# Kernel optimization log

Measured on AMD Instinct MI355X. Metric: run time of the kernel, lower is better.

Reference implementation:

```python
import jax, jax.numpy as jnp
import numpy as np

CHANNELS = 256
HEADS = 8
GROUPS = 32
EPS = 1e-5


def setup_inputs() -> dict:
    key = jax.random.key(0)
    ks = jax.random.split(key, 9)
    c = CHANNELS
    s = 1.0 / np.sqrt(c)
    return {
        "x": jax.random.normal(ks[0], (2, c, 64, 64), dtype=jnp.float32),
        "gn_w": jnp.ones((c,), jnp.float32),
        "gn_b": jnp.zeros((c,), jnp.float32),
        "qkv_w": jax.random.normal(ks[1], (3 * c, c), jnp.float32) * s,
        "qkv_b": jnp.zeros((3 * c,), jnp.float32),
        "proj_w": jax.random.normal(ks[2], (c, c), jnp.float32) * s,
        "proj_b": jnp.zeros((c,), jnp.float32),
        "gproj_w": jax.random.normal(ks[3], (c, c), jnp.float32) * s,
        "gproj_b": jnp.zeros((c,), jnp.float32),
    }


def reference(x, gn_w, gn_b, qkv_w, qkv_b, proj_w, proj_b, gproj_w, gproj_b):
    b, c, h, w = x.shape
    n = h * w
    hd = c // HEADS
    scale = hd ** (-0.5)

    # GroupNorm(32, c)
    xg = x.reshape(b, GROUPS, -1)
    mu = jnp.mean(xg, axis=-1, keepdims=True)
    var = jnp.mean((xg - mu) ** 2, axis=-1, keepdims=True)
    xn = ((xg - mu) * jax.lax.rsqrt(var + EPS)).reshape(b, c, h, w)
    xn = xn * gn_w[None, :, None, None] + gn_b[None, :, None, None]

    # global context: AdaptiveAvgPool2d(1) + 1x1 conv -> [b, c]
    gfeat = jnp.mean(xn, axis=(2, 3))                      # [b, c]
    gfeat = gfeat @ gproj_w.T + gproj_b                    # [b, c]

    # qkv 1x1 conv
    qkv = jnp.einsum('bchw,oc->bohw', xn, qkv_w) + qkv_b[None, :, None, None]
    q, k, v = qkv[:, :c], qkv[:, c:2 * c], qkv[:, 2 * c:]

    q = q.reshape(b, HEADS, hd, n).transpose(0, 1, 3, 2)   # [b,H,N,d]
    k = k.reshape(b, HEADS, hd, n) + gfeat.reshape(b, HEADS, hd, 1) * 0.1  # [b,H,d,N]
    v = v.reshape(b, HEADS, hd, n).transpose(0, 1, 3, 2)   # [b,H,N,d]

    attn = jax.nn.softmax(jnp.einsum('bhnd,bhdm->bhnm', q, k) * scale, axis=-1)
    out = jnp.einsum('bhnm,bhmd->bhnd', attn, v)           # [b,H,N,d]
    out = out.transpose(0, 1, 3, 2).reshape(b, c, h, w)

    out = jnp.einsum('bchw,oc->bohw', out, proj_w) + proj_b[None, :, None, None]
    out = out + gfeat[:, :, None, None] * 0.1
    return out + x
```

## Files before the change

kernel.cpp:

```cpp
#include <hip/hip_runtime.h>
#include <hip/hip_bf16.h>
#include <stdint.h>

#define BATCH 2
#define CH 256
#define NSP 4096
#define HEADS 8
#define HD 32
#define GROUPS 32
#define EPS_GN 1e-5f
#define NSPLIT 4

#define ATT_SCALE (0.17677669529663687f * 1.4426950408889634f)

typedef __attribute__((ext_vector_type(8))) short short8;
typedef __attribute__((ext_vector_type(4))) float f32x4;
typedef __attribute__((ext_vector_type(16))) float f32x16;
typedef __attribute__((ext_vector_type(2))) float f32x2;

#define ZERO16 ((f32x16){0.f,0.f,0.f,0.f,0.f,0.f,0.f,0.f,0.f,0.f,0.f,0.f,0.f,0.f,0.f,0.f})

static __device__ __forceinline__ unsigned short f2bf(float f) {
    union { float f; unsigned u; } v; v.f = f;
    unsigned r = v.u + 0x7fffu + ((v.u >> 16) & 1u);
    return (unsigned short)(r >> 16);
}
static __device__ __forceinline__ unsigned pkbf(float x, float y) {
    __hip_bfloat162 h = __float22bfloat162_rn(make_float2(x, y));
    return *(unsigned*)&h;
}

__global__ void k_gnstats(const float* __restrict__ x, float* __restrict__ stats) {
    int bg = blockIdx.x;
    int t = threadIdx.x;
    const float4* b4 = (const float4*)(x + (size_t)bg * (8 * NSP));
    float s = 0.f, sq = 0.f;
    #pragma unroll
    for (int i = 0; i < 32; i++) {
        float4 v = b4[t + i * 256];
        s  += v.x + v.y + v.z + v.w;
        sq += v.x * v.x + v.y * v.y + v.z * v.z + v.w * v.w;
    }
    #pragma unroll
    for (int off = 32; off > 0; off >>= 1) {
        s  += __shfl_down(s, off);
        sq += __shfl_down(sq, off);
    }
    __shared__ float rs[4], rq[4];
    int w = t >> 6;
    if ((t & 63) == 0) { rs[w] = s; rq[w] = sq; }
    __syncthreads();
    if (t == 0) {
        float S = rs[0] + rs[1] + rs[2] + rs[3];
        float Q = rq[0] + rq[1] + rq[2] + rq[3];
        float mu  = S * (1.0f / 32768.0f);
        float var = Q * (1.0f / 32768.0f) - mu * mu;
        stats[bg * 2]     = mu;
        stats[bg * 2 + 1] = rsqrtf(var + EPS_GN);
    }
}

__global__ void k_gnapply(const float* __restrict__ x, const float* __restrict__ gn_w,
                          const float* __restrict__ gn_b, const float* __restrict__ stats,
                          unsigned short* __restrict__ xnt, float* __restrict__ gpart) {
    int p0 = blockIdx.x * 64, c0 = blockIdx.y * 64, b = blockIdx.z;
    int t = threadIdx.x;
    __shared__ float tile[64][65];
    int ci0 = t >> 4, pq = t & 15;
    #pragma unroll
    for (int k = 0; k < 4; k++) {
        int ci = ci0 + k * 16;
        int c = c0 + ci;
        float mu   = stats[(b * GROUPS + (c >> 3)) * 2];
        float rstd = stats[(b * GROUPS + (c >> 3)) * 2 + 1];
        float w  = gn_w[c] * rstd;
        float bb = gn_b[c] - mu * w;
        float4 v = *(const float4*)(x + ((size_t)(b * CH + c)) * NSP + p0 + pq * 4);
        tile[ci][pq * 4 + 0] = v.x * w + bb;
        tile[ci][pq * 4 + 1] = v.y * w + bb;
        tile[ci][pq * 4 + 2] = v.z * w + bb;
        tile[ci][pq * 4 + 3] = v.w * w + bb;
    }
    __syncthreads();
    int pi = t >> 2, cb = (t & 3) * 16;
    unsigned pack[8];
    #pragma unroll
    for (int e = 0; e < 8; e++) {
        float a  = tile[cb + 2 * e][pi];
        float bv = tile[cb + 2 * e + 1][pi];
        pack[e] = (unsigned)f2bf(a) | ((unsigned)f2bf(bv) << 16);
    }
    uint4* dst = (uint4*)(xnt + ((size_t)(b * NSP + p0 + pi)) * CH + c0 + cb);
    dst[0] = make_uint4(pack[0], pack[1], pack[2], pack[3]);
    dst[1] = make_uint4(pack[4], pack[5], pack[6], pack[7]);
    if (t < 64) {
        float s = 0.f;
        #pragma unroll
        for (int j = 0; j < 64; j++) s += tile[t][j];
        gpart[((size_t)(b * CH + c0 + t)) * 64 + blockIdx.x] = s;
    }
}

__global__ void k_gproj(const float* __restrict__ gpart, const float* __restrict__ gproj_w,
                        const float* __restrict__ gproj_b, float* __restrict__ gfeat) {
    int b = blockIdx.x, t = threadIdx.x;
    __shared__ float graw[256];
    const float* p = gpart + ((size_t)(b * CH + t)) * 64;
    float s = 0.f;
    #pragma unroll
    for (int i = 0; i < 64; i++) s += p[i];
    graw[t] = s * (1.0f / 4096.0f);
    __syncthreads();
    float acc = gproj_b[t];
    const float* wr = gproj_w + (size_t)t * CH;
    #pragma unroll 8
    for (int c = 0; c < 256; c++) acc += graw[c] * wr[c];
    gfeat[b * CH + t] = acc;
}

__global__ void k_convert(const float* __restrict__ qkv_w, const float* __restrict__ proj_w,
                          unsigned short* __restrict__ wbf) {
    int i4 = blockIdx.x * 256 + threadIdx.x;
    const float* src = (i4 < 49152) ? (qkv_w + (size_t)i4 * 4)
                                    : (proj_w + (size_t)(i4 - 49152) * 4);
    float4 v = *(const float4*)src;
    ushort4 o;
    o.x = f2bf(v.x); o.y = f2bf(v.y); o.z = f2bf(v.z); o.w = f2bf(v.w);
    *(ushort4*)(wbf + (size_t)i4 * 4) = o;
}

__global__ void k_gemm_qkv(const unsigned short* __restrict__ Ag,
                           const unsigned short* __restrict__ Btg,
                           const float* __restrict__ bias,
                           const float* __restrict__ gfeat,
                           unsigned short* __restrict__ qt,
                           unsigned short* __restrict__ kt,
                           unsigned short* __restrict__ vt) {
    int n0 = blockIdx.x * 128, m0 = blockIdx.y * 64, b = blockIdx.z;
    int t = threadIdx.x, lane = t & 63, w = t >> 6;
    int wm = w >> 1, wn = w & 1;
    __shared__ short A_lds[64][40];
    __shared__ short B_lds[128][40];
    const unsigned short* Bb = Btg + (size_t)b * NSP * CH;
    f32x4 acc[2][4];
    #pragma unroll
    for (int m = 0; m < 2; m++)
        #pragma unroll
        for (int n = 0; n < 4; n++) acc[m][n] = (f32x4){0.f, 0.f, 0.f, 0.f};
    int arow = t >> 2, akk = (t & 3) * 8;
    for (int k0 = 0; k0 < 256; k0 += 32) {
        __syncthreads();
        *(uint4*)&A_lds[arow][akk] = *(const uint4*)(Ag + (size_t)(m0 + arow) * CH + k0 + akk);
        #pragma unroll
        for (int hh = 0; hh < 2; hh++) {
            int f = t + hh * 256;
            int j = f >> 2, kk = (f & 3) * 8;
            *(uint4*)&B_lds[j][kk] = *(const uint4*)(Bb + (size_t)(n0 + j) * CH + k0 + kk);
        }
        __syncthreads();
        short8 a[2], bf[4];
        #pragma unroll
        for (int m = 0; m < 2; m++)
            a[m] = *(const short8*)&A_lds[wm * 32 + m * 16 + (lane & 15)][(lane >> 4) * 8];
        #pragma unroll
        for (int n = 0; n < 4; n++)
            bf[n] = *(const short8*)&B_lds[wn * 64 + n * 16 + (lane & 15)][(lane >> 4) * 8];
        #pragma unroll
        for (int m = 0; m < 2; m++)
            #pragma unroll
            for (int n = 0; n < 4; n++)
                acc[m][n] = __builtin_amdgcn_mfma_f32_16x16x32_bf16(a[m], bf[n], acc[m][n], 0, 0, 0);
    }
    int rbase = m0 + wm * 32 + ((lane >> 4) << 2);
    int cbase = n0 + wn * 64 + (lane & 15);
    #pragma unroll
    for (int m = 0; m < 2; m++) {
        int row0 = rbase + m * 16;
        int sec = row0 >> 8;
        int ch  = row0 & 255;
        int h = ch >> 5, d0 = ch & 31;
        #pragma unroll
        for (int n = 0; n < 4; n++) {
            int col = cbase + n * 16;
            if (sec == 0) {
                ushort4 pk;
                pk.x = f2bf(acc[m][n][0] + bias[row0 + 0]);
                pk.y = f2bf(acc[m][n][1] + bias[row0 + 1]);
                pk.z = f2bf(acc[m][n][2] + bias[row0 + 2]);
                pk.w = f2bf(acc[m][n][3] + bias[row0 + 3]);
                *(ushort4*)(qt + ((size_t)((b * 8 + h) * NSP + col)) * HD + d0) = pk;
            } else if (sec == 1) {
                ushort4 pk;
                #pragma unroll
                for (int i = 0; i < 4; i++) {
                    float v = (acc[m][n][i] + bias[row0 + i]
                               + 0.1f * gfeat[b * CH + ch + i]) * ATT_SCALE;
                    ((unsigned short*)&pk)[i] = f2bf(v);
                }
                *(ushort4*)(kt + ((size_t)((b * 8 + h) * NSP + col)) * HD + d0) = pk;
            } else {
                #pragma unroll
                for (int i = 0; i < 4; i++) {
                    float v = acc[m][n][i] + bias[row0 + i];
                    vt[((size_t)((b * 8 + h) * HD + d0 + i)) * NSP + col] = f2bf(v);
                }
            }
        }
    }
}

__global__ void k_gemm_proj(const unsigned short* __restrict__ Ag,
                            const unsigned short* __restrict__ Btg,
                            const float* __restrict__ bias,
                            const float* __restrict__ gfeat,
                            const float* __restrict__ xres,
                            float* __restrict__ out) {
    int n0 = blockIdx.x * 128, m0 = blockIdx.y * 64, b = blockIdx.z;
    int t = threadIdx.x, lane = t & 63, w = t >> 6;
    int wm = w >> 1, wn = w & 1;
    __shared__ short A_lds[64][40];
    __shared__ short B_lds[128][40];
    const unsigned short* Bb = Btg + (size_t)b * NSP * CH;
    f32x4 acc[2][4];
    #pragma unroll
    for (int m = 0; m < 2; m++)
        #pragma unroll
        for (int n = 0; n < 4; n++) acc[m][n] = (f32x4){0.f, 0.f, 0.f, 0.f};
    int arow = t >> 2, akk = (t & 3) * 8;
    for (int k0 = 0; k0 < 256; k0 += 32) {
        __syncthreads();
        *(uint4*)&A_lds[arow][akk] = *(const uint4*)(Ag + (size_t)(m0 + arow) * CH + k0 + akk);
        #pragma unroll
        for (int hh = 0; hh < 2; hh++) {
            int f = t + hh * 256;
            int j = f >> 2, kk = (f & 3) * 8;
            *(uint4*)&B_lds[j][kk] = *(const uint4*)(Bb + (size_t)(n0 + j) * CH + k0 + kk);
        }
        __syncthreads();
        short8 a[2], bf[4];
        #pragma unroll
        for (int m = 0; m < 2; m++)
            a[m] = *(const short8*)&A_lds[wm * 32 + m * 16 + (lane & 15)][(lane >> 4) * 8];
        #pragma unroll
        for (int n = 0; n < 4; n++)
            bf[n] = *(const short8*)&B_lds[wn * 64 + n * 16 + (lane & 15)][(lane >> 4) * 8];
        #pragma unroll
        for (int m = 0; m < 2; m++)
            #pragma unroll
            for (int n = 0; n < 4; n++)
                acc[m][n] = __builtin_amdgcn_mfma_f32_16x16x32_bf16(a[m], bf[n], acc[m][n], 0, 0, 0);
    }
    int rbase = m0 + wm * 32 + ((lane >> 4) << 2);
    int cbase = n0 + wn * 64 + (lane & 15);
    #pragma unroll
    for (int m = 0; m < 2; m++) {
        #pragma unroll
        for (int n = 0; n < 4; n++) {
            int col = cbase + n * 16;
            #pragma unroll
            for (int i = 0; i < 4; i++) {
                int row = rbase + m * 16 + i;
                float add = bias[row] + 0.1f * gfeat[b * CH + row]
                          + xres[((size_t)(b * CH + row)) * NSP + col];
                out[((size_t)(b * CH + row)) * NSP + col] = acc[m][n][i] + add;
            }
        }
    }
}

__global__ __launch_bounds__(256, 8)
void k_flash32(const unsigned short* __restrict__ qt,
               const unsigned short* __restrict__ kt,
               const unsigned short* __restrict__ vt,
               unsigned short* __restrict__ opart, float* __restrict__ lpart) {
    const int h = blockIdx.y, b = blockIdx.z;
    const int s = blockIdx.x >> 5;
    const int t = threadIdx.x, lane = t & 63, w = t >> 6;
    const int lo32 = lane & 31, hi = lane >> 5;
    const int q0 = (blockIdx.x & 31) * 128 + w * 32;
    const int j0base = s * (NSP / NSPLIT);
    const unsigned short* qp = qt + ((size_t)(b * 8 + h) * NSP) * HD;
    const unsigned short* kp = kt + ((size_t)(b * 8 + h) * NSP) * HD;
    const unsigned short* vp = vt + ((size_t)(b * 8 + h) * HD) * NSP;
    __shared__ __align__(16) unsigned short K_lds[64 * 40];
    __shared__ __align__(16) unsigned short V_lds[32 * 64];

    short8 qf0 = *(const short8*)(qp + (size_t)(q0 + lo32) * HD + hi * 8);
    short8 qf1 = *(const short8*)(qp + (size_t)(q0 + lo32) * HD + 16 + hi * 8);
    f32x16 oacc;
    #pragma unroll
    for (int i = 0; i < 16; i++) oacc[i] = 0.f;
    float l = 0.f;

    const int krow = (t & 7) + 8 * (t >> 5);
    const int kslot = (t >> 3) & 3;
    const int vd = t >> 3, vslot = t & 7;
    const unsigned short* kga = kp + (size_t)(j0base + krow) * HD + kslot * 8;
    const unsigned short* vga = vp + (size_t)vd * NSP + j0base + vslot * 8;
    const int kws = krow * 40 + kslot * 8;
    const int vws = vd * 64 + ((vslot ^ (vd & 7)) * 8);

    const int NT = NSP / NSPLIT / 64;
    for (int it = 0; it < NT; ++it) {
        {
            uint4 kreg = *(const uint4*)(kga + (size_t)it * 64 * HD);
            uint4 vreg = *(const uint4*)(vga + it * 64);
            *(uint4*)&K_lds[kws] = kreg;
            *(uint4*)&V_lds[vws] = vreg;
        }
        __syncthreads();
        #pragma unroll
        for (int hf = 0; hf < 2; hf++) {
            const int jj = hf * 32 + lo32;
            short8 kf0 = *(const short8*)&K_lds[jj * 40 + hi * 8];
            short8 kf1 = *(const short8*)&K_lds[jj * 40 + (2 + hi) * 8];
            f32x16 sv;
            __builtin_amdgcn_s_setprio(1);
            sv = __builtin_amdgcn_mfma_f32_32x32x16_bf16(kf0, qf0, ZERO16, 0, 0, 0);
            sv = __builtin_amdgcn_mfma_f32_32x32x16_bf16(kf1, qf1, sv, 0, 0, 0);
            __builtin_amdgcn_s_setprio(0);
            #pragma unroll
            for (int i = 0; i < 16; i++) sv[i] = __builtin_amdgcn_exp2f(sv[i]);
            {
                #define SH2(V, I) __builtin_shufflevector(V, V, 2*(I), 2*(I)+1)
                f32x2 t0 = (SH2(sv,0) + SH2(sv,1)) + (SH2(sv,2) + SH2(sv,3));
                f32x2 t1 = (SH2(sv,4) + SH2(sv,5)) + (SH2(sv,6) + SH2(sv,7));
                f32x2 tt = t0 + t1;
                float sm = tt[0] + tt[1];
                #undef SH2
                unsigned sb = __builtin_bit_cast(unsigned, sm);
                auto sx = __builtin_amdgcn_permlane32_swap(sb, sb, false, false);
                l += __builtin_bit_cast(float, (unsigned)sx[0])
                   + __builtin_bit_cast(float, (unsigned)sx[1]);
            }
            #define PVSTEP(SV, BB, C) { \
                unsigned p0 = pkbf(SV[BB + 0], SV[BB + 1]); \
                unsigned p1 = pkbf(SV[BB + 2], SV[BB + 3]); \
                unsigned p2 = pkbf(SV[BB + 4], SV[BB + 5]); \
                unsigned p3 = pkbf(SV[BB + 6], SV[BB + 7]); \
                auto s02 = __builtin_amdgcn_permlane32_swap(p0, p2, false, false); \
                auto s13 = __builtin_amdgcn_permlane32_swap(p1, p3, false, false); \
                uint4 fu = make_uint4((unsigned)s02[0], (unsigned)s13[0], \
                                      (unsigned)s02[1], (unsigned)s13[1]); \
                short8 pa = *(short8*)&fu; \
                short8 vf = *(const short8*)&V_lds[lo32 * 64 + ((((C) * 2 + hi) ^ (lo32 & 7)) * 8)]; \
                oacc = __builtin_amdgcn_mfma_f32_32x32x16_bf16(vf, pa, oacc, 0, 0, 0); \
            }
            __builtin_amdgcn_s_setprio(1);
            PVSTEP(sv, 0, hf * 2)
            PVSTEP(sv, 8, hf * 2 + 1)
            __builtin_amdgcn_s_setprio(0);
            #undef PVSTEP
        }
        __syncthreads();
    }
    unsigned short* op = opart + ((((size_t)s * BATCH + b) * HEADS + h) * NSP + q0 + lo32) * HD;
    #pragma unroll
    for (int rr = 0; rr < 4; rr++) {
        ushort4 pk4;
        pk4.x = f2bf(oacc[rr * 4 + 0]);
        pk4.y = f2bf(oacc[rr * 4 + 1]);
        pk4.z = f2bf(oacc[rr * 4 + 2]);
        pk4.w = f2bf(oacc[rr * 4 + 3]);
        *(ushort4*)(op + rr * 8 + hi * 4) = pk4;
    }
    if (hi == 0)
        lpart[(((size_t)s * BATCH + b) * HEADS + h) * NSP + q0 + lo32] = l;
}

__global__ __launch_bounds__(256)
void k_combine(const unsigned short* __restrict__ opart, const float* __restrict__ lpart,
               unsigned short* __restrict__ att) {
    int flat = blockIdx.x * 256 + threadIdx.x;
    int dchunk = flat & 3;
    int q = (flat >> 2) & (NSP - 1);
    int bh = flat >> 14;
    const size_t sO = (size_t)BATCH * HEADS * NSP * HD;
    const size_t sL = (size_t)BATCH * HEADS * NSP;
    size_t rowq = (size_t)bh * NSP + q;
    float den = 0.f;
    #pragma unroll
    for (int s2 = 0; s2 < NSPLIT; s2++) den += lpart[s2 * sL + rowq];
    float inv = 1.0f / den;
    float acc[8];
    #pragma unroll
    for (int e = 0; e < 8; e++) acc[e] = 0.f;
    #pragma unroll
    for (int s2 = 0; s2 < NSPLIT; s2++) {
        uint4 v = *(const uint4*)(opart + s2 * sO + rowq * HD + dchunk * 8);
        const unsigned short* pv = (const unsigned short*)&v;
        #pragma unroll
        for (int e = 0; e < 8; e++) {
            unsigned u = (unsigned)pv[e] << 16;
            acc[e] += *(float*)&u;
        }
    }
    uint4 o;
    o.x = (unsigned)f2bf(acc[0] * inv) | ((unsigned)f2bf(acc[1] * inv) << 16);
    o.y = (unsigned)f2bf(acc[2] * inv) | ((unsigned)f2bf(acc[3] * inv) << 16);
    o.z = (unsigned)f2bf(acc[4] * inv) | ((unsigned)f2bf(acc[5] * inv) << 16);
    o.w = (unsigned)f2bf(acc[6] * inv) | ((unsigned)f2bf(acc[7] * inv) << 16);
    *(uint4*)(att + ((size_t)((bh >> 3) * NSP + q)) * CH + (bh & 7) * HD + dchunk * 8) = o;
}

extern "C" void kernel_launch(void* const* d_in, const int* in_sizes, int n_in,
                              void* d_out, int out_size, void* d_ws, size_t ws_size,
                              hipStream_t stream) {
    const float* x       = (const float*)d_in[0];
    const float* gn_w    = (const float*)d_in[1];
    const float* gn_b    = (const float*)d_in[2];
    const float* qkv_w   = (const float*)d_in[3];
    const float* qkv_b   = (const float*)d_in[4];
    const float* proj_w  = (const float*)d_in[5];
    const float* proj_b  = (const float*)d_in[6];
    const float* gproj_w = (const float*)d_in[7];
    const float* gproj_b = (const float*)d_in[8];
    char* ws = (char*)d_ws;
    float*          stats  = (float*)(ws);
    float*          gpart  = (float*)(ws + 1024);
    float*          gfeat  = (float*)(ws + 132096);
    unsigned short* wbf    = (unsigned short*)(ws + 134144);
    unsigned short* xnt    = (unsigned short*)(ws + 658432);
    float*          lpart  = (float*)(ws + 658432);
    unsigned short* qt     = (unsigned short*)(ws + 4852736);
    unsigned short* kt     = (unsigned short*)(ws + 9047040);
    unsigned short* vt     = (unsigned short*)(ws + 13241344);
    unsigned short* att    = (unsigned short*)(ws + 17435648);
    unsigned short* opart  = (unsigned short*)(ws + 21629952);
    float* out = (float*)d_out;

    hipLaunchKernelGGL(k_gnstats, dim3(64), dim3(256), 0, stream, x, stats);
    hipLaunchKernelGGL(k_gnapply, dim3(64, 4, 2), dim3(256), 0, stream,
                       x, gn_w, gn_b, stats, xnt, gpart);
    hipLaunchKernelGGL(k_gproj, dim3(2), dim3(256), 0, stream,
                       gpart, gproj_w, gproj_b, gfeat);
    hipLaunchKernelGGL(k_convert, dim3(256), dim3(256), 0, stream, qkv_w, proj_w, wbf);
    hipLaunchKernelGGL(k_gemm_qkv, dim3(32, 12, 2), dim3(256), 0, stream,
                       wbf, xnt, qkv_b, gfeat, qt, kt, vt);
    hipLaunchKernelGGL(k_flash32, dim3(32 * NSPLIT, 8, 2), dim3(256), 0, stream,
                       qt, kt, vt, opart, lpart);
    hipLaunchKernelGGL(k_combine, dim3(1024), dim3(256), 0, stream,
                       opart, lpart, att);
    hipLaunchKernelGGL(k_gemm_proj, dim3(32, 4, 2), dim3(256), 0, stream,
                       wbf + 196608, att, proj_b, gfeat, x, out);
}
```

Measured before the change: 111.8 us.

## Fuse split-softmax combine into projection GEMM and pad V tile in LDS

After: 109.9 us. No clear change (-1.7%).

```diff
diff --git a/kernel.cpp b/kernel.cpp
--- a/kernel.cpp
+++ b/kernel.cpp
@@ -24,6 +24,10 @@
     union { float f; unsigned u; } v; v.f = f;
     unsigned r = v.u + 0x7fffu + ((v.u >> 16) & 1u);
     return (unsigned short)(r >> 16);
+}
+static __device__ __forceinline__ float bf2f(unsigned short u) {
+    unsigned v = (unsigned)u << 16;
+    return *(float*)&v;
 }
 static __device__ __forceinline__ unsigned pkbf(float x, float y) {
     __hip_bfloat162 h = __float22bfloat162_rn(make_float2(x, y));
@@ -210,7 +214,8 @@
 }
 
 __global__ void k_gemm_proj(const unsigned short* __restrict__ Ag,
-                            const unsigned short* __restrict__ Btg,
+                            const unsigned short* __restrict__ opart,
+                            const float* __restrict__ lpart,
                             const float* __restrict__ bias,
                             const float* __restrict__ gfeat,
                             const float* __restrict__ xres,
@@ -220,7 +225,7 @@
     int wm = w >> 1, wn = w & 1;
     __shared__ short A_lds[64][40];
     __shared__ short B_lds[128][40];
-    const unsigned short* Bb = Btg + (size_t)b * NSP * CH;
+    const size_t sO = (size_t)BATCH * HEADS * NSP;
     f32x4 acc[2][4];
     #pragma unroll
     for (int m = 0; m < 2; m++)
@@ -230,11 +235,33 @@
     for (int k0 = 0; k0 < 256; k0 += 32) {
         __syncthreads();
         *(uint4*)&A_lds[arow][akk] = *(const uint4*)(Ag + (size_t)(m0 + arow) * CH + k0 + akk);
+        int hidx = k0 >> 5;
         #pragma unroll
         for (int hh = 0; hh < 2; hh++) {
             int f = t + hh * 256;
             int j = f >> 2, kk = (f & 3) * 8;
-            *(uint4*)&B_lds[j][kk] = *(const uint4*)(Bb + (size_t)(n0 + j) * CH + k0 + kk);
+            size_t rowq = ((size_t)(b * HEADS + hidx)) * NSP + n0 + j;
+            float den = 0.f;
+            float a0 = 0.f, a1 = 0.f, a2 = 0.f, a3 = 0.f,
+                  a4 = 0.f, a5 = 0.f, a6 = 0.f, a7 = 0.f;
+            #pragma unroll
+            for (int s2 = 0; s2 < NSPLIT; s2++) {
+                size_t off = (size_t)s2 * sO + rowq;
+                den += lpart[off];
+                uint4 v = *(const uint4*)(opart + off * HD + kk);
+                const unsigned short* pv = (const unsigned short*)&v;
+                a0 += bf2f(pv[0]); a1 += bf2f(pv[1]);
+                a2 += bf2f(pv[2]); a3 += bf2f(pv[3]);
+                a4 += bf2f(pv[4]); a5 += bf2f(pv[5]);
+                a6 += bf2f(pv[6]); a7 += bf2f(pv[7]);
+            }
+            float inv = 1.0f / den;
+            uint4 pk;
+            pk.x = (unsigned)f2bf(a0 * inv) | ((unsigned)f2bf(a1 * inv) << 16);
+            pk.y = (unsigned)f2bf(a2 * inv) | ((unsigned)f2bf(a3 * inv) << 16);
+            pk.z = (unsigned)f2bf(a4 * inv) | ((unsigned)f2bf(a5 * inv) << 16);
+            pk.w = (unsigned)f2bf(a6 * inv) | ((unsigned)f2bf(a7 * inv) << 16);
+            *(uint4*)&B_lds[j][kk] = pk;
         }
         __syncthreads();
         short8 a[2], bf[4];
@@ -283,7 +310,7 @@
     const unsigned short* kp = kt + ((size_t)(b * 8 + h) * NSP) * HD;
     const unsigned short* vp = vt + ((size_t)(b * 8 + h) * HD) * NSP;
     __shared__ __align__(16) unsigned short K_lds[64 * 40];
-    __shared__ __align__(16) unsigned short V_lds[32 * 64];
+    __shared__ __align__(16) unsigned short V_lds[32 * 68];
 
     short8 qf0 = *(const short8*)(qp + (size_t)(q0 + lo32) * HD + hi * 8);
     short8 qf1 = *(const short8*)(qp + (size_t)(q0 + lo32) * HD + 16 + hi * 8);
@@ -298,7 +325,7 @@
     const unsigned short* kga = kp + (size_t)(j0base + krow) * HD + kslot * 8;
     const unsigned short* vga = vp + (size_t)vd * NSP + j0base + vslot * 8;
     const int kws = krow * 40 + kslot * 8;
-    const int vws = vd * 64 + ((vslot ^ (vd & 7)) * 8);
+    const int vws = vd * 68 + vslot * 8;
 
     const int NT = NSP / NSPLIT / 64;
     for (int it = 0; it < NT; ++it) {
@@ -343,7 +370,7 @@
                 uint4 fu = make_uint4((unsigned)s02[0], (unsigned)s13[0], \
                                       (unsigned)s02[1], (unsigned)s13[1]); \
                 short8 pa = *(short8*)&fu; \
-                short8 vf = *(const short8*)&V_lds[lo32 * 64 + ((((C) * 2 + hi) ^ (lo32 & 7)) * 8)]; \
+                short8 vf = *(const short8*)&V_lds[lo32 * 68 + ((C) * 2 + hi) * 8]; \
                 oacc = __builtin_amdgcn_mfma_f32_32x32x16_bf16(vf, pa, oacc, 0, 0, 0); \
             }
             __builtin_amdgcn_s_setprio(1);
@@ -366,41 +393,6 @@
     }
     if (hi == 0)
         lpart[(((size_t)s * BATCH + b) * HEADS + h) * NSP + q0 + lo32] = l;
-}
-
-__global__ __launch_bounds__(256)
-void k_combine(const unsigned short* __restrict__ opart, const float* __restrict__ lpart,
-               unsigned short* __restrict__ att) {
-    int flat = blockIdx.x * 256 + threadIdx.x;
-    int dchunk = flat & 3;
-    int q = (flat >> 2) & (NSP - 1);
-    int bh = flat >> 14;
-    const size_t sO = (size_t)BATCH * HEADS * NSP * HD;
-    const size_t sL = (size_t)BATCH * HEADS * NSP;
-    size_t rowq = (size_t)bh * NSP + q;
-    float den = 0.f;
-    #pragma unroll
-    for (int s2 = 0; s2 < NSPLIT; s2++) den += lpart[s2 * sL + rowq];
-    float inv = 1.0f / den;
-    float acc[8];
-    #pragma unroll
-    for (int e = 0; e < 8; e++) acc[e] = 0.f;
-    #pragma unroll
-    for (int s2 = 0; s2 < NSPLIT; s2++) {
-        uint4 v = *(const uint4*)(opart + s2 * sO + rowq * HD + dchunk * 8);
-        const unsigned short* pv = (const unsigned short*)&v;
-        #pragma unroll
-        for (int e = 0; e < 8; e++) {
-            unsigned u = (unsigned)pv[e] << 16;
-            acc[e] += *(float*)&u;
-        }
-    }
-    uint4 o;
-    o.x = (unsigned)f2bf(acc[0] * inv) | ((unsigned)f2bf(acc[1] * inv) << 16);
-    o.y = (unsigned)f2bf(acc[2] * inv) | ((unsigned)f2bf(acc[3] * inv) << 16);
-    o.z = (unsigned)f2bf(acc[4] * inv) | ((unsigned)f2bf(acc[5] * inv) << 16);
-    o.w = (unsigned)f2bf(acc[6] * inv) | ((unsigned)f2bf(acc[7] * inv) << 16);
-    *(uint4*)(att + ((size_t)((bh >> 3) * NSP + q)) * CH + (bh & 7) * HD + dchunk * 8) = o;
 }
 
 extern "C" void kernel_launch(void* const* d_in, const int* in_sizes, int n_in,
@@ -425,7 +417,6 @@
     unsigned short* qt     = (unsigned short*)(ws + 4852736);
     unsigned short* kt     = (unsigned short*)(ws + 9047040);
     unsigned short* vt     = (unsigned short*)(ws + 13241344);
-    unsigned short* att    = (unsigned short*)(ws + 17435648);
     unsigned short* opart  = (unsigned short*)(ws + 21629952);
     float* out = (float*)d_out;
 
@@ -439,8 +430,6 @@
                        wbf, xnt, qkv_b, gfeat, qt, kt, vt);
     hipLaunchKernelGGL(k_flash32, dim3(32 * NSPLIT, 8, 2), dim3(256), 0, stream,
                        qt, kt, vt, opart, lpart);
-    hipLaunchKernelGGL(k_combine, dim3(1024), dim3(256), 0, stream,
-                       opart, lpart, att);
     hipLaunchKernelGGL(k_gemm_proj, dim3(32, 4, 2), dim3(256), 0, stream,
-                       wbf + 196608, att, proj_b, gfeat, x, out);
-}
+                       wbf + 196608, opart, lpart, proj_b, gfeat, x, out);
+}
```
